# Kernel optimization log

Measured on AMD Instinct MI355X. Metric: run time of the kernel, lower is better.

## Reference

```python
import jax, jax.numpy as jnp
import numpy as np

B, S, T, H, NH, NL = 16, 128, 64, 128, 8, 4
DH = H // NH
FF = 2 * H
SCALE = 1.0 / float(np.sqrt(DH))


def _ln(x, s, b):
    m = x.mean(-1, keepdims=True)
    v = ((x - m) ** 2).mean(-1, keepdims=True)
    return (x - m) * jax.lax.rsqrt(v + 1e-5) * s + b


def _block(x, mask, p):
    Wq, bq, Wk, bk, Wv, bv, Wo, bo, s1, c1, W1, d1, W2, d2, s2, c2 = p
    N, L, _ = x.shape
    q = (x @ Wq + bq).reshape(N, L, NH, DH)
    k = (x @ Wk + bk).reshape(N, L, NH, DH)
    v = (x @ Wv + bv).reshape(N, L, NH, DH)
    scores = jnp.einsum('nqhd,nkhd->nhqk', q, k) * SCALE
    scores = jnp.where(mask[:, None, :, :], scores, -1e9)
    a = jax.nn.softmax(scores, axis=-1)
    o = jnp.einsum('nhqk,nkhd->nqhd', a, v).reshape(N, L, H)
    x = _ln(x + o @ Wo + bo, s1, c1)
    h = jax.nn.relu(x @ W1 + d1)
    return _ln(x + h @ W2 + d2, s2, c2)


def setup_inputs():
    key = jax.random.key(0)
    ks = jax.random.split(key, 16)
    g = lambda k, shape: jax.random.normal(k, shape, jnp.float32) * 0.02
    return {
        'polylines': jax.random.normal(ks[0], (B, S, T, H), jnp.float32),
        'lengths': jax.random.randint(ks[1], (B, S), 0, T + 1),
        'proj_w': g(ks[2], (H, H)), 'proj_b': jnp.zeros((H,), jnp.float32),
        'proj_ln_s': jnp.ones((H,), jnp.float32), 'proj_ln_b': jnp.zeros((H,), jnp.float32),
        'pos_emb': g(ks[3], (1, T, H)),
        'Wq': g(ks[4], (NL, H, H)), 'bq': jnp.zeros((NL, H), jnp.float32),
        'Wk': g(ks[5], (NL, H, H)), 'bk': jnp.zeros((NL, H), jnp.float32),
        'Wv': g(ks[6], (NL, H, H)), 'bv': jnp.zeros((NL, H), jnp.float32),
        'Wo': g(ks[7], (NL, H, H)), 'bo': jnp.zeros((NL, H), jnp.float32),
        'ln1_s': jnp.ones((NL, H), jnp.float32), 'ln1_b': jnp.zeros((NL, H), jnp.float32),
        'W1': g(ks[8], (NL, H, FF)), 'b1': jnp.zeros((NL, FF), jnp.float32),
        'W2': g(ks[9], (NL, FF, H)), 'b2': jnp.zeros((NL, H), jnp.float32),
        'ln2_s': jnp.ones((NL, H), jnp.float32), 'ln2_b': jnp.zeros((NL, H), jnp.float32),
    }


def reference(polylines, lengths, proj_w, proj_b, proj_ln_s, proj_ln_b, pos_emb,
              Wq, bq, Wk, bk, Wv, bv, Wo, bo, ln1_s, ln1_b, W1, b1, W2, b2, ln2_s, ln2_b):
    # valid[b,s,t] = t < lengths[b,s]; lengths==0 -> polyline absent (fully padded)
    valid = jnp.arange(T)[None, None, :] < lengths[:, :, None]  # [B,S,T]
    x = jnp.where(valid[..., None], polylines, -1.0)            # -1 pad as in np.pad(constant_values=-1)
    # mask_temporal[b,s] = outer(valid[b,s], valid[b,s])
    mask_t = (valid[:, :, :, None] & valid[:, :, None, :]).reshape(B * S, T, T)
    # mask_spatial[b,t] = outer(valid[b,:,t], valid[b,:,t])
    vs = jnp.transpose(valid, (0, 2, 1))                        # [B,T,S]
    mask_s = (vs[:, :, :, None] & vs[:, :, None, :]).reshape(B * T, S, S)

    x = x.reshape(B * S, T, H)
    x = jax.nn.relu(_ln(x @ proj_w + proj_b, proj_ln_s, proj_ln_b))  # MLP: Linear->LN->ReLU
    x = x + pos_emb[:, :T, :]

    mask = mask_t
    for i in range(NL):
        if i == NL // 2:
            # switch from temporal to spatial attention: [B*S,T,H] -> [B*T,S,H]
            x = x.reshape(B, S, T, H).transpose(0, 2, 1, 3).reshape(B * T, S, H)
            mask = mask_s
        p = (Wq[i], bq[i], Wk[i], bk[i], Wv[i], bv[i], Wo[i], bo[i],
             ln1_s[i], ln1_b[i], W1[i], b1[i], W2[i], b2[i], ln2_s[i], ln2_b[i])
        x = _block(x, mask, p)
    # faithful to original final reshape (treats [B*T,S,H] buffer as [B,S,T,H])
    return x.reshape(B, S, T, H)[:, 0, :]
```

## Files before the change

### kernel.cpp

```cpp
#include <hip/hip_runtime.h>

typedef short short8 __attribute__((ext_vector_type(8)));
typedef short short4_t __attribute__((ext_vector_type(4)));
typedef float floatx4 __attribute__((ext_vector_type(4)));
typedef unsigned short ushort_t;

#define B_ 16
#define S_ 128
#define T_ 64
#define H_ 128
#define FF_ 256
#define SCALEQK 0.25f

#define OFFP 0
#define OFFQ(l) (16384 + (l) * 65536)
#define OFFK(l) (OFFQ(l) + 16384)
#define OFFV(l) (OFFQ(l) + 32768)
#define OFFO(l) (OFFQ(l) + 49152)
#define OFFW1(l) (278528 + (l) * 65536)
#define OFFW2(l) (OFFW1(l) + 32768)

__device__ __forceinline__ float b2f(ushort_t u) {
    union { unsigned int i; float f; } x; x.i = ((unsigned int)u) << 16; return x.f;
}
__device__ __forceinline__ ushort_t f2b(float f) {
    union { float f; unsigned int i; } x; x.f = f;
    unsigned int r = x.i + 0x7fffu + ((x.i >> 16) & 1u);
    return (ushort_t)(r >> 16);
}
__device__ __forceinline__ int pack2b(float a, float b) {
    return (int)f2b(a) | ((int)f2b(b) << 16);
}

struct WtEnt { const float* src; int N; int K; int nclog2; int dstoff; };
struct WtArgs { WtEnt e[25]; };

__global__ __launch_bounds__(256) void wt_kernel(WtArgs a, ushort_t* __restrict__ dst) {
    WtEnt ent = a.e[blockIdx.x];
    const int tiles_c = ent.N >> 5;
    const int nt = (ent.K >> 5) * tiles_c;
    const int t = blockIdx.y;
    if (t >= nt) return;
    const int tc = t & (tiles_c - 1);
    const int tr = t >> ent.nclog2;
    __shared__ float ld[32 * 33];
    const int tid = threadIdx.x;
#pragma unroll
    for (int i = 0; i < 4; ++i) {
        int e = tid + i * 256;
        int rr = e >> 5, cc = e & 31;
        ld[rr * 33 + cc] = ent.src[(tr * 32 + rr) * ent.N + tc * 32 + cc];
    }
    __syncthreads();
    ushort_t* d = dst + ent.dstoff;
#pragma unroll
    for (int i = 0; i < 4; ++i) {
        int e = tid + i * 256;
        int rr = e >> 5, cc = e & 31;
        d[(tc * 32 + rr) * ent.K + tr * 32 + cc] = f2b(ld[cc * 33 + rr]);
    }
}

template<int RT, int CT, int KK>
__device__ __forceinline__ void mm_g(const ushort_t* aL, int sa,
                                     const ushort_t* __restrict__ wT,
                                     int colbase, int lane, floatx4 (&acc)[RT][CT]) {
    const int l15 = lane & 15, lq8 = (lane >> 4) * 8;
#pragma unroll
    for (int r = 0; r < RT; ++r)
#pragma unroll
        for (int c = 0; c < CT; ++c) acc[r][c] = (floatx4){0.f, 0.f, 0.f, 0.f};
#pragma unroll
    for (int k0 = 0; k0 < KK; k0 += 32) {
        short8 b[CT];
#pragma unroll
        for (int c = 0; c < CT; ++c)
            b[c] = *(const short8*)&wT[(colbase + c * 16 + l15) * KK + k0 + lq8];
#pragma unroll
        for (int r = 0; r < RT; ++r) {
            short8 a = *(const short8*)&aL[(r * 16 + l15) * sa + k0 + lq8];
#pragma unroll
            for (int c = 0; c < CT; ++c)
                acc[r][c] = __builtin_amdgcn_mfma_f32_16x16x32_bf16(a, b[c], acc[r][c], 0, 0, 0);
        }
    }
}

template<int RT, int CT>
__device__ __forceinline__ void add_bias(floatx4 (&acc)[RT][CT], const float* b,
                                         int colbase, int l15) {
#pragma unroll
    for (int c = 0; c < CT; ++c) {
        float bc = b[colbase + c * 16 + l15];
#pragma unroll
        for (int r = 0; r < RT; ++r)
#pragma unroll
            for (int g = 0; g < 4; ++g) acc[r][c][g] += bc;
    }
}

template<int RT, int CT>
__device__ __forceinline__ void add_resid_reg(floatx4 (&acc)[RT][CT],
                                              const float (&res)[RT][CT][4]) {
#pragma unroll
    for (int r = 0; r < RT; ++r)
#pragma unroll
        for (int c = 0; c < CT; ++c)
#pragma unroll
            for (int g = 0; g < 4; ++g) acc[r][c][g] += res[r][c][g];
}
template<int RT, int CT>
__device__ __forceinline__ void save_resid(float (&res)[RT][CT][4],
                                           const floatx4 (&acc)[RT][CT]) {
#pragma unroll
    for (int r = 0; r < RT; ++r)
#pragma unroll
        for (int c = 0; c < CT; ++c)
#pragma unroll
            for (int g = 0; g < 4; ++g) res[r][c][g] = acc[r][c][g];
}

template<int RT, int CT>
__device__ __forceinline__ void st_n(const floatx4 (&acc)[RT][CT], ushort_t* dst, int stride,
                                     int colbase, int l15, int lq) {
#pragma unroll
    for (int r = 0; r < RT; ++r)
#pragma unroll
        for (int g = 0; g < 4; ++g) {
            int row = r * 16 + lq * 4 + g;
#pragma unroll
            for (int c = 0; c < CT; ++c)
                dst[row * stride + colbase + c * 16 + l15] = f2b(acc[r][c][g]);
        }
}

template<int RT, int CT>
__device__ __forceinline__ void st_t(const floatx4 (&acc)[RT][CT], ushort_t* dst, int stride,
                                     int colbase, int l15, int lq) {
#pragma unroll
    for (int r = 0; r < RT; ++r)
#pragma unroll
        for (int c = 0; c < CT; ++c) {
            int d = colbase + c * 16 + l15;
            short4_t p;
#pragma unroll
            for (int g = 0; g < 4; ++g) p[g] = (short)f2b(acc[r][c][g]);
            *(short4_t*)&dst[d * stride + r * 16 + lq * 4] = p;
        }
}

template<int RT, int CT>
__device__ __forceinline__ void ln_norm(floatx4 (&acc)[RT][CT], float* redL,
                                        const float* lns, const float* lnb,
                                        int colbase, int l15, int lq, int wv) {
#pragma unroll
    for (int r = 0; r < RT; ++r)
#pragma unroll
        for (int g = 0; g < 4; ++g) {
            float s = 0.f, q = 0.f;
#pragma unroll
            for (int c = 0; c < CT; ++c) { float v = acc[r][c][g]; s += v; q += v * v; }
            s += __shfl_xor(s, 1); s += __shfl_xor(s, 2); s += __shfl_xor(s, 4); s += __shfl_xor(s, 8);
            q += __shfl_xor(q, 1); q += __shfl_xor(q, 2); q += __shfl_xor(q, 4); q += __shfl_xor(q, 8);
            if (l15 == 0) {
                int row = r * 16 + lq * 4 + g;
                redL[row * 8 + wv] = s;
                redL[row * 8 + 4 + wv] = q;
            }
        }
    __syncthreads();
#pragma unroll
    for (int r = 0; r < RT; ++r)
#pragma unroll
        for (int g = 0; g < 4; ++g) {
            int row = r * 16 + lq * 4 + g;
            float4 S = *(float4*)&redL[row * 8];
            float4 Q = *(float4*)&redL[row * 8 + 4];
            float mean = (S.x + S.y + S.z + S.w) * (1.f / 128.f);
            float var = (Q.x + Q.y + Q.z + Q.w) * (1.f / 128.f) - mean * mean;
            float rstd = rsqrtf(var + 1e-5f);
#pragma unroll
            for (int c = 0; c < CT; ++c) {
                int col = colbase + c * 16 + l15;
                acc[r][c][g] = (acc[r][c][g] - mean) * rstd * lns[col] + lnb[col];
            }
        }
}

template<int JT>
__device__ __forceinline__ void softmax_pack(floatx4 (&st)[JT], bool iv, unsigned jm,
                                             int (&px)[JT][2]) {
    float ev[JT][4];
    float mx = -3.0e38f;
#pragma unroll
    for (int jt = 0; jt < JT; ++jt)
#pragma unroll
        for (int g = 0; g < 4; ++g) {
            bool ok = iv && ((jm >> (jt * 4 + g)) & 1u);
            float s = ok ? st[jt][g] * SCALEQK : -1e9f;
            ev[jt][g] = s; mx = fmaxf(mx, s);
        }
    mx = fmaxf(mx, __shfl_xor(mx, 16)); mx = fmaxf(mx, __shfl_xor(mx, 32));
    float sum = 0.f;
#pragma unroll
    for (int jt = 0; jt < JT; ++jt)
#pragma unroll
        for (int g = 0; g < 4; ++g) { float e = __expf(ev[jt][g] - mx); ev[jt][g] = e; sum += e; }
    sum += __shfl_xor(sum, 16); sum += __shfl_xor(sum, 32);
    float inv = 1.f / sum;
#pragma unroll
    for (int jt = 0; jt < JT; ++jt) {
        px[jt][0] = pack2b(ev[jt][0] * inv, ev[jt][1] * inv);
        px[jt][1] = pack2b(ev[jt][2] * inv, ev[jt][3] * inv);
    }
}

__device__ __forceinline__ short8 pfrag(const int (*px)[2], int jc, int lq, int l15) {
    const int jA = (lq & 1) * 32 + l15;
    int a0 = __shfl(px[jc * 2][0], jA);
    int a1 = __shfl(px[jc * 2][1], jA);
    int a2 = __shfl(px[jc * 2][0], jA + 16);
    int a3 = __shfl(px[jc * 2][1], jA + 16);
    int b0 = __shfl(px[jc * 2 + 1][0], jA);
    int b1 = __shfl(px[jc * 2 + 1][1], jA);
    int b2 = __shfl(px[jc * 2 + 1][0], jA + 16);
    int b3 = __shfl(px[jc * 2 + 1][1], jA + 16);
    const bool t = (lq >> 1) != 0;
    union { int4 i; short8 s; } u;
    u.i = make_int4(t ? b0 : a0, t ? b1 : a1, t ? b2 : a2, t ? b3 : a3);
    return u.s;
}
__device__ __forceinline__ short8 vfrag(const ushort_t* vT, int stride, int row, int off) {
    int2 a = *(const int2*)&vT[row * stride + off];
    int2 b = *(const int2*)&vT[row * stride + off + 4];
    union { int4 i; short8 s; } u;
    u.i = make_int4(a.x, a.y, b.x, b.y);
    return u.s;
}

__global__ __launch_bounds__(256, 2) void k1_mega(
    const float* __restrict__ poly, const int* __restrict__ lens,
    const ushort_t* __restrict__ wt,
    const float* __restrict__ projb, const float* __restrict__ pls,
    const float* __restrict__ plb, const float* __restrict__ pos,
    const float* __restrict__ bq0, const float* __restrict__ bk0,
    const float* __restrict__ bv0, const float* __restrict__ bo0,
    const float* __restrict__ l1s0, const float* __restrict__ l1b0,
    const float* __restrict__ b10, const float* __restrict__ b20,
    const float* __restrict__ l2s0, const float* __restrict__ l2b0,
    const float* __restrict__ bq1, const float* __restrict__ bk1,
    const float* __restrict__ bv1,
    ushort_t* __restrict__ o1, float* __restrict__ xr0f)
{
    __shared__ ushort_t pool[34816];
    __shared__ float redL[512];
    __shared__ float psL[8 * 68];
    __shared__ float q1L[128];
    ushort_t* xL = pool;
    ushort_t* qL = pool + 8704;
    ushort_t* kL = pool + 17408;
    ushort_t* vT = pool + 26112;
    ushort_t* hL = pool + 17408;

    const int tid = threadIdx.x, lane = tid & 63, wv = tid >> 6;
    const int l15 = lane & 15, lq = lane >> 4;
    const int g = blockIdx.x;
    const int len = lens[g];

    {
        const float* pg = poly + (size_t)g * 8192;
#pragma unroll
        for (int it = 0; it < 8; ++it) {
            int e4 = (tid + it * 256) * 4;
            int row = e4 >> 7, col = e4 & 127;
            float4 f = *(const float4*)(pg + e4);
            if (row >= len) { f.x = -1.f; f.y = -1.f; f.z = -1.f; f.w = -1.f; }
            short4_t u;
            u[0] = (short)f2b(f.x); u[1] = (short)f2b(f.y);
            u[2] = (short)f2b(f.z); u[3] = (short)f2b(f.w);
            *(short4_t*)&xL[row * 136 + col] = u;
        }
    }
    __syncthreads();

    floatx4 a2[4][2];
    float xre[4][2][4];

    mm_g<4, 2, 128>(xL, 136, wt + OFFP, wv * 32, lane, a2);
    add_bias<4, 2>(a2, projb, wv * 32, l15);
    ln_norm<4, 2>(a2, redL, pls, plb, wv * 32, l15, lq, wv);
    __syncthreads();
#pragma unroll
    for (int r = 0; r < 4; ++r)
#pragma unroll
        for (int gg = 0; gg < 4; ++gg) {
            int row = r * 16 + lq * 4 + gg;
#pragma unroll
            for (int c = 0; c < 2; ++c) {
                int col = wv * 32 + c * 16 + l15;
                float v = fmaxf(a2[r][c][gg], 0.f) + pos[row * 128 + col];
                xre[r][c][gg] = v;
                xL[row * 136 + col] = f2b(v);
            }
        }
    __syncthreads();

    mm_g<4, 2, 128>(xL, 136, wt + OFFQ(0), wv * 32, lane, a2);
    add_bias<4, 2>(a2, bq0, wv * 32, l15);
    st_n<4, 2>(a2, qL, 136, wv * 32, l15, lq);
    mm_g<4, 2, 128>(xL, 136, wt + OFFK(0), wv * 32, lane, a2);
    add_bias<4, 2>(a2, bk0, wv * 32, l15);
    st_n<4, 2>(a2, kL, 136, wv * 32, l15, lq);
    mm_g<4, 2, 128>(xL, 136, wt + OFFV(0), wv * 32, lane, a2);
    add_bias<4, 2>(a2, bv0, wv * 32, l15);
    st_t<4, 2>(a2, vT, 68, wv * 32, l15, lq);
    __syncthreads();

    {
        const int iRow = wv * 16 + l15;
        const bool iv = iRow < len;
        unsigned jm = 0;
#pragma unroll
        for (int jt = 0; jt < 4; ++jt)
#pragma unroll
            for (int gg = 0; gg < 4; ++gg)
                if (jt * 16 + lq * 4 + gg < len) jm |= (1u << (jt * 4 + gg));
        for (int h = 0; h < 8; ++h) {
            const int hc = h * 16;
            short8 z8 = {0, 0, 0, 0, 0, 0, 0, 0};
            short8 bqf = z8;
            if (lq < 2) bqf = *(const short8*)&qL[iRow * 136 + hc + lq * 8];
            floatx4 st[4];
#pragma unroll
            for (int jt = 0; jt < 4; ++jt) {
                short8 ak = z8;
                if (lq < 2) ak = *(const short8*)&kL[(jt * 16 + l15) * 136 + hc + lq * 8];
                floatx4 zz = {0.f, 0.f, 0.f, 0.f};
                st[jt] = __builtin_amdgcn_mfma_f32_16x16x32_bf16(ak, bqf, zz, 0, 0, 0);
            }
            int px[4][2];
            softmax_pack<4>(st, iv, jm, px);
            floatx4 ao = {0.f, 0.f, 0.f, 0.f};
#pragma unroll
            for (int jc = 0; jc < 2; ++jc) {
                short8 av = vfrag(vT, 68, hc + l15, jc * 32 + lq * 8);
                short8 bp = pfrag(px, jc, lq, l15);
                ao = __builtin_amdgcn_mfma_f32_16x16x32_bf16(av, bp, ao, 0, 0, 0);
            }
            short4_t w;
#pragma unroll
            for (int gg = 0; gg < 4; ++gg) w[gg] = (short)f2b(ao[gg]);
            *(short4_t*)&qL[iRow * 136 + hc + lq * 4] = w;
        }
    }
    __syncthreads();

    mm_g<4, 2, 128>(qL, 136, wt + OFFO(0), wv * 32, lane, a2);
    add_bias<4, 2>(a2, bo0, wv * 32, l15);
    add_resid_reg<4, 2>(a2, xre);
    ln_norm<4, 2>(a2, redL, l1s0, l1b0, wv * 32, l15, lq, wv);
    save_resid<4, 2>(xre, a2);
    st_n<4, 2>(a2, xL, 136, wv * 32, l15, lq);
    __syncthreads();

    {
        floatx4 a4[4][4];
        mm_g<4, 4, 128>(xL, 136, wt + OFFW1(0), wv * 64, lane, a4);
        add_bias<4, 4>(a4, b10, wv * 64, l15);
#pragma unroll
        for (int r = 0; r < 4; ++r)
#pragma unroll
            for (int c = 0; c < 4; ++c)
#pragma unroll
                for (int gg = 0; gg < 4; ++gg) a4[r][c][gg] = fmaxf(a4[r][c][gg], 0.f);
        st_n<4, 4>(a4, hL, 272, wv * 64, l15, lq);
    }
    __syncthreads();

    mm_g<4, 2, 256>(hL, 272, wt + OFFW2(0), wv * 32, lane, a2);
    add_bias<4, 2>(a2, b20, wv * 32, l15);
    add_resid_reg<4, 2>(a2, xre);
    ln_norm<4, 2>(a2, redL, l2s0, l2b0, wv * 32, l15, lq, wv);
    save_resid<4, 2>(xre, a2);
    st_n<4, 2>(a2, xL, 136, wv * 32, l15, lq);
    if (lq == 0) {
#pragma unroll
        for (int c = 0; c < 2; ++c)
            xr0f[(size_t)g * 128 + wv * 32 + c * 16 + l15] = a2[0][c][0];
    }
    __syncthreads();

    mm_g<4, 2, 128>(xL, 136, wt + OFFK(1), wv * 32, lane, a2);
    add_bias<4, 2>(a2, bk1, wv * 32, l15);
    st_n<4, 2>(a2, kL, 136, wv * 32, l15, lq);
    mm_g<4, 2, 128>(xL, 136, wt + OFFV(1), wv * 32, lane, a2);
    add_bias<4, 2>(a2, bv1, wv * 32, l15);
    st_t<4, 2>(a2, vT, 68, wv * 32, l15, lq);
    if (tid < 128) {
        int d = tid;
        float a = bq1[d];
        const ushort_t* wq = wt + OFFQ(1) + d * 128;
#pragma unroll 4
        for (int j0 = 0; j0 < 128; j0 += 8) {
            short8 w8 = *(const short8*)&wq[j0];
            short8 x8 = *(const short8*)&xL[j0];
#pragma unroll
            for (int q = 0; q < 8; ++q)
                a = fmaf(b2f((ushort_t)x8[q]), b2f((ushort_t)w8[q]), a);
        }
        q1L[d] = a;
    }
    __syncthreads();

    {
        int h = tid >> 5, jj = tid & 31;
        int hc = h * 16;
        float s[2];
#pragma unroll
        for (int half = 0; half < 2; ++half) {
            int j = jj + half * 32;
            float a = 0.f;
            short8 k0v = *(const short8*)&kL[j * 136 + hc];
            short8 k1v = *(const short8*)&kL[j * 136 + hc + 8];
#pragma unroll
            for (int q = 0; q < 8; ++q) {
                a = fmaf(q1L[hc + q], b2f((ushort_t)k0v[q]), a);
                a = fmaf(q1L[hc + 8 + q], b2f((ushort_t)k1v[q]), a);
            }
            s[half] = (j < len) ? a * SCALEQK : -1e9f;
        }
        float mx = fmaxf(s[0], s[1]);
#pragma unroll
        for (int d = 1; d < 32; d <<= 1) mx = fmaxf(mx, __shfl_xor(mx, d));
        float e0 = __expf(s[0] - mx), e1 = __expf(s[1] - mx);
        float sum = e0 + e1;
#pragma unroll
        for (int d = 1; d < 32; d <<= 1) sum += __shfl_xor(sum, d);
        float inv = 1.f / sum;
        psL[h * 68 + jj] = e0 * inv;
        psL[h * 68 + jj + 32] = e1 * inv;
    }
    __syncthreads();
    if (tid < 128) {
        int h = tid >> 4, d = tid & 15, hc = h * 16;
        float a = 0.f;
#pragma unroll 4
        for (int j0 = 0; j0 < 64; j0 += 4) {
            float4 p4 = *(const float4*)&psL[h * 68 + j0];
            short4_t v4 = *(const short4_t*)&vT[(hc + d) * 68 + j0];
            a += p4.x * b2f((ushort_t)v4[0]) + p4.y * b2f((ushort_t)v4[1])
               + p4.z * b2f((ushort_t)v4[2]) + p4.w * b2f((ushort_t)v4[3]);
        }
        o1[(size_t)g * 128 + hc + d] = f2b(a);
    }
}

__global__ __launch_bounds__(256, 1) void k2_tail(
    const int* __restrict__ lens, const ushort_t* __restrict__ wt,
    const ushort_t* __restrict__ o1, const float* __restrict__ xr0f,
    const float* __restrict__ bq, const float* __restrict__ bk,
    const float* __restrict__ bv, const float* __restrict__ bo,
    const float* __restrict__ l1s, const float* __restrict__ l1b,
    const float* __restrict__ b1, const float* __restrict__ b2,
    const float* __restrict__ l2s, const float* __restrict__ l2b,
    float* __restrict__ outp)
{
    __shared__ ushort_t pool[69632];
    __shared__ float redL[1024];
    __shared__ int vld[128];
    ushort_t* yL = pool;
    ushort_t* qL = pool + 17408;
    ushort_t* kL = pool + 34816;
    ushort_t* vT = pool + 52224;
    ushort_t* hL = pool + 34816;

    const int tid = threadIdx.x, lane = tid & 63, wv = tid >> 6;
    const int l15 = lane & 15, lq = lane >> 4;
    const int b = blockIdx.x;

    if (tid < 128) vld[tid] = (lens[b * 128 + tid] > 0) ? 1 : 0;
#pragma unroll
    for (int it = 0; it < 8; ++it) {
        int e = tid + it * 256;
        int row = e >> 4, cg = e & 15;
        *(short8*)&kL[row * 136 + cg * 8] =
            *(const short8*)&o1[((size_t)b * 128 + row) * 128 + cg * 8];
    }
    __syncthreads();

    floatx4 a2[8][2];
    float yre[8][2][4];

    mm_g<8, 2, 128>(kL, 136, wt + OFFO(1), wv * 32, lane, a2);
    add_bias<8, 2>(a2, bo + 128, wv * 32, l15);
#pragma unroll
    for (int r = 0; r < 8; ++r)
#pragma unroll
        for (int gg = 0; gg < 4; ++gg) {
            int row = r * 16 + lq * 4 + gg;
#pragma unroll
            for (int c = 0; c < 2; ++c)
                a2[r][c][gg] += xr0f[((size_t)b * 128 + row) * 128 + wv * 32 + c * 16 + l15];
        }
    ln_norm<8, 2>(a2, redL, l1s + 128, l1b + 128, wv * 32, l15, lq, wv);
    save_resid<8, 2>(yre, a2);
    st_n<8, 2>(a2, yL, 136, wv * 32, l15, lq);
    __syncthreads();
    {
        floatx4 a4[8][4];
        mm_g<8, 4, 128>(yL, 136, wt + OFFW1(1), wv * 64, lane, a4);
        add_bias<8, 4>(a4, b1 + FF_, wv * 64, l15);
#pragma unroll
        for (int r = 0; r < 8; ++r)
#pragma unroll
            for (int c = 0; c < 4; ++c)
#pragma unroll
                for (int gg = 0; gg < 4; ++gg) a4[r][c][gg] = fmaxf(a4[r][c][gg], 0.f);
        st_n<8, 4>(a4, hL, 272, wv * 64, l15, lq);
    }
    __syncthreads();
    mm_g<8, 2, 256>(hL, 272, wt + OFFW2(1), wv * 32, lane, a2);
    add_bias<8, 2>(a2, b2 + 128, wv * 32, l15);
    add_resid_reg<8, 2>(a2, yre);
    ln_norm<8, 2>(a2, redL, l2s + 128, l2b + 128, wv * 32, l15, lq, wv);
    save_resid<8, 2>(yre, a2);
    st_n<8, 2>(a2, yL, 136, wv * 32, l15, lq);
    __syncthreads();

    unsigned jm = 0;
#pragma unroll
    for (int jt = 0; jt < 8; ++jt)
#pragma unroll
        for (int gg = 0; gg < 4; ++gg)
            if (vld[jt * 16 + lq * 4 + gg]) jm |= (1u << (jt * 4 + gg));
    const int i0 = wv * 32 + l15, i1 = i0 + 16;
    const bool iv0 = vld[i0] != 0, iv1 = vld[i1] != 0;

    for (int l = 2; l < 4; ++l) {
        mm_g<8, 2, 128>(yL, 136, wt + OFFQ(l), wv * 32, lane, a2);
        add_bias<8, 2>(a2, bq + l * 128, wv * 32, l15);
        st_n<8, 2>(a2, qL, 136, wv * 32, l15, lq);
        mm_g<8, 2, 128>(yL, 136, wt + OFFK(l), wv * 32, lane, a2);
        add_bias<8, 2>(a2, bk + l * 128, wv * 32, l15);
        st_n<8, 2>(a2, kL, 136, wv * 32, l15, lq);
        mm_g<8, 2, 128>(yL, 136, wt + OFFV(l), wv * 32, lane, a2);
        add_bias<8, 2>(a2, bv + l * 128, wv * 32, l15);
        st_t<8, 2>(a2, vT, 136, wv * 32, l15, lq);
        __syncthreads();
        for (int h = 0; h < 8; ++h) {
            const int hc = h * 16;
            short8 z8 = {0, 0, 0, 0, 0, 0, 0, 0};
            short8 bqa = z8, bqb = z8;
            if (lq < 2) {
                bqa = *(const short8*)&qL[i0 * 136 + hc + lq * 8];
                bqb = *(const short8*)&qL[i1 * 136 + hc + lq * 8];
            }
            floatx4 s0[8], s1[8];
#pragma unroll
            for (int jt = 0; jt < 8; ++jt) {
                short8 ak = z8;
                if (lq < 2) ak = *(const short8*)&kL[(jt * 16 + l15) * 136 + hc + lq * 8];
                floatx4 zz = {0.f, 0.f, 0.f, 0.f};
                s0[jt] = __builtin_amdgcn_mfma_f32_16x16x32_bf16(ak, bqa, zz, 0, 0, 0);
                s1[jt] = __builtin_amdgcn_mfma_f32_16x16x32_bf16(ak, bqb, zz, 0, 0, 0);
            }
            int px0[8][2], px1[8][2];
            softmax_pack<8>(s0, iv0, jm, px0);
            softmax_pack<8>(s1, iv1, jm, px1);
            floatx4 o0 = {0.f, 0.f, 0.f, 0.f}, o1a = {0.f, 0.f, 0.f, 0.f};
#pragma unroll
            for (int jc = 0; jc < 4; ++jc) {
                short8 av = vfrag(vT, 136, hc + l15, jc * 32 + lq * 8);
                o0 = __builtin_amdgcn_mfma_f32_16x16x32_bf16(av, pfrag(px0, jc, lq, l15), o0, 0, 0, 0);
                o1a = __builtin_amdgcn_mfma_f32_16x16x32_bf16(av, pfrag(px1, jc, lq, l15), o1a, 0, 0, 0);
            }
            short4_t w0, w1;
#pragma unroll
            for (int gg = 0; gg < 4; ++gg) { w0[gg] = (short)f2b(o0[gg]); w1[gg] = (short)f2b(o1a[gg]); }
            *(short4_t*)&qL[i0 * 136 + hc + lq * 4] = w0;
            *(short4_t*)&qL[i1 * 136 + hc + lq * 4] = w1;
        }
        __syncthreads();
        mm_g<8, 2, 128>(qL, 136, wt + OFFO(l), wv * 32, lane, a2);
        add_bias<8, 2>(a2, bo + l * 128, wv * 32, l15);
        add_resid_reg<8, 2>(a2, yre);
        ln_norm<8, 2>(a2, redL, l1s + l * 128, l1b + l * 128, wv * 32, l15, lq, wv);
        save_resid<8, 2>(yre, a2);
        st_n<8, 2>(a2, yL, 136, wv * 32, l15, lq);
        __syncthreads();
        {
            floatx4 a4[8][4];
            mm_g<8, 4, 128>(yL, 136, wt + OFFW1(l), wv * 64, lane, a4);
            add_bias<8, 4>(a4, b1 + l * FF_, wv * 64, l15);
#pragma unroll
            for (int r = 0; r < 8; ++r)
#pragma unroll
                for (int c = 0; c < 4; ++c)
#pragma unroll
                    for (int gg = 0; gg < 4; ++gg) a4[r][c][gg] = fmaxf(a4[r][c][gg], 0.f);
            st_n<8, 4>(a4, hL, 272, wv * 64, l15, lq);
        }
        __syncthreads();
        mm_g<8, 2, 256>(hL, 272, wt + OFFW2(l), wv * 32, lane, a2);
        add_bias<8, 2>(a2, b2 + l * 128, wv * 32, l15);
        add_resid_reg<8, 2>(a2, yre);
        ln_norm<8, 2>(a2, redL, l2s + l * 128, l2b + l * 128, wv * 32, l15, lq, wv);
        if (l == 3) {
#pragma unroll
            for (int r = 0; r < 4; ++r)
#pragma unroll
                for (int gg = 0; gg < 4; ++gg) {
                    int row = r * 16 + lq * 4 + gg;
#pragma unroll
                    for (int c = 0; c < 2; ++c)
                        outp[(size_t)b * 8192 + row * 128 + wv * 32 + c * 16 + l15] = a2[r][c][gg];
                }
        } else {
            save_resid<8, 2>(yre, a2);
            st_n<8, 2>(a2, yL, 136, wv * 32, l15, lq);
        }
        __syncthreads();
    }
}

extern "C" void kernel_launch(void* const* d_in, const int* in_sizes, int n_in,
                              void* d_out, int out_size, void* d_ws, size_t ws_size,
                              hipStream_t stream)
{
    const float* poly   = (const float*)d_in[0];
    const int*   lens   = (const int*)d_in[1];
    const float* proj_w = (const float*)d_in[2];
    const float* proj_b = (const float*)d_in[3];
    const float* pls    = (const float*)d_in[4];
    const float* plb    = (const float*)d_in[5];
    const float* pos    = (const float*)d_in[6];
    const float* Wq = (const float*)d_in[7];
    const float* bq = (const float*)d_in[8];
    const float* Wk = (const float*)d_in[9];
    const float* bk = (const float*)d_in[10];
    const float* Wv = (const float*)d_in[11];
    const float* bv = (const float*)d_in[12];
    const float* Wo = (const float*)d_in[13];
    const float* bo = (const float*)d_in[14];
    const float* l1s = (const float*)d_in[15];
    const float* l1b = (const float*)d_in[16];
    const float* W1 = (const float*)d_in[17];
    const float* b1 = (const float*)d_in[18];
    const float* W2 = (const float*)d_in[19];
    const float* b2 = (const float*)d_in[20];
    const float* l2s = (const float*)d_in[21];
    const float* l2b = (const float*)d_in[22];
    float* outp = (float*)d_out;

    char* base = (char*)d_ws;
    ushort_t* wt    = (ushort_t*)base;
    ushort_t* o1buf = (ushort_t*)(base + 1081344);
    float* xr0f     = (float*)(base + 1605632);

    const int HH = H_ * H_, HF = H_ * FF_;
    WtArgs wa;
    wa.e[0] = {proj_w, 128, 128, 2, OFFP};
    for (int l = 0; l < 4; ++l) {
        wa.e[1 + l * 4 + 0] = {Wq + l * HH, 128, 128, 2, OFFQ(l)};
        wa.e[1 + l * 4 + 1] = {Wk + l * HH, 128, 128, 2, OFFK(l)};
        wa.e[1 + l * 4 + 2] = {Wv + l * HH, 128, 128, 2, OFFV(l)};
        wa.e[1 + l * 4 + 3] = {Wo + l * HH, 128, 128, 2, OFFO(l)};
    }
    for (int l = 0; l < 4; ++l) {
        wa.e[17 + l * 2 + 0] = {W1 + l * HF, 256, 128, 3, OFFW1(l)};
        wa.e[17 + l * 2 + 1] = {W2 + l * HF, 128, 256, 2, OFFW2(l)};
    }
    wt_kernel<<<dim3(25, 32), 256, 0, stream>>>(wa, wt);

    k1_mega<<<dim3(2048), 256, 0, stream>>>(
        poly, lens, wt,
        proj_b, pls, plb, pos,
        bq, bk, bv, bo, l1s, l1b, b1, b2, l2s, l2b,
        bq + H_, bk + H_, bv + H_,
        o1buf, xr0f);

    k2_tail<<<dim3(16), 256, 0, stream>>>(
        lens, wt, o1buf, xr0f,
        bq, bk, bv, bo, l1s, l1b, b1, b2, l2s, l2b,
        outp);
}
```

Baseline: 471.6 us.

## Prefetch next weight fragments into registers across GEMMs in tail kernel

The 16-block tail kernel now loads each wave's B-operand weight fragments for the next GEMM into registers (double-buffered cur/nxt) while the current GEMM runs on MFMA. The FF GEMMs are split into 128-column and 128-deep chunks so each chunk uses the same fragment shape. This targets global-memory latency on weight loads in a latency-bound kernel with very few blocks. In exchange it needs many more VGPRs (two 8x short8 fragment sets plus accumulators), which could cause spills.

New measurement: 496.3 us. 1.05x slower.

```diff
diff --git a/kernel.cpp b/kernel.cpp
--- a/kernel.cpp
+++ b/kernel.cpp
@@ -236,6 +236,47 @@
     union { int4 i; short8 s; } u;
     u.i = make_int4(a.x, a.y, b.x, b.y);
     return u.s;
+}
+
+struct BFrag { short8 b[8]; };
+__device__ __forceinline__ void ld_bf(BFrag& f, const ushort_t* __restrict__ wT,
+                                      int KK, int colbase, int koff, int lane) {
+    const int l15 = lane & 15, lq8 = (lane >> 4) * 8;
+#pragma unroll
+    for (int c = 0; c < 2; ++c)
+#pragma unroll
+        for (int k = 0; k < 4; ++k)
+            f.b[c * 4 + k] =
+                *(const short8*)&wT[(size_t)(colbase + c * 16 + l15) * KK + koff + k * 32 + lq8];
+}
+template<bool INIT>
+__device__ __forceinline__ void mm_c(const ushort_t* aL, int sa, int aoff,
+                                     const BFrag& f, int lane, floatx4 (&acc)[8][2]) {
+    const int l15 = lane & 15, lq8 = (lane >> 4) * 8;
+    if (INIT) {
+#pragma unroll
+        for (int r = 0; r < 8; ++r)
+#pragma unroll
+            for (int c = 0; c < 2; ++c) acc[r][c] = (floatx4){0.f, 0.f, 0.f, 0.f};
+    }
+#pragma unroll
+    for (int k0 = 0; k0 < 4; ++k0)
+#pragma unroll
+        for (int r = 0; r < 8; ++r) {
+            short8 a = *(const short8*)&aL[(r * 16 + l15) * sa + aoff + k0 * 32 + lq8];
+#pragma unroll
+            for (int c = 0; c < 2; ++c)
+                acc[r][c] = __builtin_amdgcn_mfma_f32_16x16x32_bf16(a, f.b[c * 4 + k0], acc[r][c], 0, 0, 0);
+        }
+}
+template<int RT, int CT>
+__device__ __forceinline__ void relu_a(floatx4 (&acc)[RT][CT]) {
+#pragma unroll
+    for (int r = 0; r < RT; ++r)
+#pragma unroll
+        for (int c = 0; c < CT; ++c)
+#pragma unroll
+            for (int g = 0; g < 4; ++g) acc[r][c][g] = fmaxf(acc[r][c][g], 0.f);
 }
 
 __global__ __launch_bounds__(256, 2) void k1_mega(
@@ -264,11 +305,11 @@
 
     const int tid = threadIdx.x, lane = tid & 63, wv = tid >> 6;
     const int l15 = lane & 15, lq = lane >> 4;
-    const int g = blockIdx.x;
-    const int len = lens[g];
+    const int gid = blockIdx.x;
+    const int len = lens[gid];
 
     {
-        const float* pg = poly + (size_t)g * 8192;
+        const float* pg = poly + (size_t)gid * 8192;
 #pragma unroll
         for (int it = 0; it < 8; ++it) {
             int e4 = (tid + it * 256) * 4;
@@ -367,12 +408,7 @@
         floatx4 a4[4][4];
         mm_g<4, 4, 128>(xL, 136, wt + OFFW1(0), wv * 64, lane, a4);
         add_bias<4, 4>(a4, b10, wv * 64, l15);
-#pragma unroll
-        for (int r = 0; r < 4; ++r)
-#pragma unroll
-            for (int c = 0; c < 4; ++c)
-#pragma unroll
-                for (int gg = 0; gg < 4; ++gg) a4[r][c][gg] = fmaxf(a4[r][c][gg], 0.f);
+        relu_a<4, 4>(a4);
         st_n<4, 4>(a4, hL, 272, wv * 64, l15, lq);
     }
     __syncthreads();
@@ -386,7 +422,7 @@
     if (lq == 0) {
 #pragma unroll
         for (int c = 0; c < 2; ++c)
-            xr0f[(size_t)g * 128 + wv * 32 + c * 16 + l15] = a2[0][c][0];
+            xr0f[(size_t)gid * 128 + wv * 32 + c * 16 + l15] = a2[0][c][0];
     }
     __syncthreads();
 
@@ -451,11 +487,11 @@
             a += p4.x * b2f((ushort_t)v4[0]) + p4.y * b2f((ushort_t)v4[1])
                + p4.z * b2f((ushort_t)v4[2]) + p4.w * b2f((ushort_t)v4[3]);
         }
-        o1[(size_t)g * 128 + hc + d] = f2b(a);
-    }
-}
-
-__global__ __launch_bounds__(256, 1) void k2_tail(
+        o1[(size_t)gid * 128 + hc + d] = f2b(a);
+    }
+}
+
+__global__ __launch_bounds__(256, 1) void k2_pipe(
     const int* __restrict__ lens, const ushort_t* __restrict__ wt,
     const ushort_t* __restrict__ o1, const float* __restrict__ xr0f,
     const float* __restrict__ bq, const float* __restrict__ bk,
@@ -477,6 +513,10 @@
     const int tid = threadIdx.x, lane = tid & 63, wv = tid >> 6;
     const int l15 = lane & 15, lq = lane >> 4;
     const int b = blockIdx.x;
+    const int cb = wv * 32;
+
+    BFrag cur, nxt;
+    ld_bf(cur, wt + OFFO(1), 128, cb, 0, lane);
 
     if (tid < 128) vld[tid] = (lens[b * 128 + tid] > 0) ? 1 : 0;
 #pragma unroll
@@ -491,8 +531,9 @@
     floatx4 a2[8][2];
     float yre[8][2][4];
 
-    mm_g<8, 2, 128>(kL, 136, wt + OFFO(1), wv * 32, lane, a2);
-    add_bias<8, 2>(a2, bo + 128, wv * 32, l15);
+    ld_bf(nxt, wt + OFFW1(1), 128, cb, 0, lane);
+    mm_c<true>(kL, 136, 0, cur, lane, a2);
+    add_bias<8, 2>(a2, bo + H_, cb, l15);
 #pragma unroll
     for (int r = 0; r < 8; ++r)
 #pragma unroll
@@ -500,32 +541,39 @@
             int row = r * 16 + lq * 4 + gg;
 #pragma unroll
             for (int c = 0; c < 2; ++c)
-                a2[r][c][gg] += xr0f[((size_t)b * 128 + row) * 128 + wv * 32 + c * 16 + l15];
-        }
-    ln_norm<8, 2>(a2, redL, l1s + 128, l1b + 128, wv * 32, l15, lq, wv);
+                a2[r][c][gg] += xr0f[((size_t)b * 128 + row) * 128 + cb + c * 16 + l15];
+        }
+    ln_norm<8, 2>(a2, redL, l1s + H_, l1b + H_, cb, l15, lq, wv);
     save_resid<8, 2>(yre, a2);
-    st_n<8, 2>(a2, yL, 136, wv * 32, l15, lq);
-    __syncthreads();
-    {
-        floatx4 a4[8][4];
-        mm_g<8, 4, 128>(yL, 136, wt + OFFW1(1), wv * 64, lane, a4);
-        add_bias<8, 4>(a4, b1 + FF_, wv * 64, l15);
-#pragma unroll
-        for (int r = 0; r < 8; ++r)
-#pragma unroll
-            for (int c = 0; c < 4; ++c)
-#pragma unroll
-                for (int gg = 0; gg < 4; ++gg) a4[r][c][gg] = fmaxf(a4[r][c][gg], 0.f);
-        st_n<8, 4>(a4, hL, 272, wv * 64, l15, lq);
-    }
-    __syncthreads();
-    mm_g<8, 2, 256>(hL, 272, wt + OFFW2(1), wv * 32, lane, a2);
-    add_bias<8, 2>(a2, b2 + 128, wv * 32, l15);
+    st_n<8, 2>(a2, yL, 136, cb, l15, lq);
+    __syncthreads();
+    cur = nxt;
+
+    ld_bf(nxt, wt + OFFW1(1), 128, 128 + cb, 0, lane);
+    mm_c<true>(yL, 136, 0, cur, lane, a2);
+    add_bias<8, 2>(a2, b1 + FF_, cb, l15);
+    relu_a<8, 2>(a2);
+    st_n<8, 2>(a2, hL, 272, cb, l15, lq);
+    cur = nxt;
+    ld_bf(nxt, wt + OFFW2(1), 256, cb, 0, lane);
+    mm_c<true>(yL, 136, 0, cur, lane, a2);
+    add_bias<8, 2>(a2, b1 + FF_, 128 + cb, l15);
+    relu_a<8, 2>(a2);
+    st_n<8, 2>(a2, hL, 272, 128 + cb, l15, lq);
+    __syncthreads();
+    cur = nxt;
+    ld_bf(nxt, wt + OFFW2(1), 256, cb, 128, lane);
+    mm_c<true>(hL, 272, 0, cur, lane, a2);
+    cur = nxt;
+    ld_bf(nxt, wt + OFFQ(2), 128, cb, 0, lane);
+    mm_c<false>(hL, 272, 128, cur, lane, a2);
+    add_bias<8, 2>(a2, b2 + H_, cb, l15);
     add_resid_reg<8, 2>(a2, yre);
-    ln_norm<8, 2>(a2, redL, l2s + 128, l2b + 128, wv * 32, l15, lq, wv);
+    ln_norm<8, 2>(a2, redL, l2s + H_, l2b + H_, cb, l15, lq, wv);
     save_resid<8, 2>(yre, a2);
-    st_n<8, 2>(a2, yL, 136, wv * 32, l15, lq);
-    __syncthreads();
+    st_n<8, 2>(a2, yL, 136, cb, l15, lq);
+    __syncthreads();
+    cur = nxt;
 
     unsigned jm = 0;
 #pragma unroll
@@ -533,20 +581,26 @@
 #pragma unroll
         for (int gg = 0; gg < 4; ++gg)
             if (vld[jt * 16 + lq * 4 + gg]) jm |= (1u << (jt * 4 + gg));
-    const int i0 = wv * 32 + l15, i1 = i0 + 16;
+    const int i0 = cb + l15, i1 = i0 + 16;
     const bool iv0 = vld[i0] != 0, iv1 = vld[i1] != 0;
 
     for (int l = 2; l < 4; ++l) {
-        mm_g<8, 2, 128>(yL, 136, wt + OFFQ(l), wv * 32, lane, a2);
-        add_bias<8, 2>(a2, bq + l * 128, wv * 32, l15);
-        st_n<8, 2>(a2, qL, 136, wv * 32, l15, lq);
-        mm_g<8, 2, 128>(yL, 136, wt + OFFK(l), wv * 32, lane, a2);
-        add_bias<8, 2>(a2, bk + l * 128, wv * 32, l15);
-        st_n<8, 2>(a2, kL, 136, wv * 32, l15, lq);
-        mm_g<8, 2, 128>(yL, 136, wt + OFFV(l), wv * 32, lane, a2);
-        add_bias<8, 2>(a2, bv + l * 128, wv * 32, l15);
-        st_t<8, 2>(a2, vT, 136, wv * 32, l15, lq);
+        ld_bf(nxt, wt + OFFK(l), 128, cb, 0, lane);
+        mm_c<true>(yL, 136, 0, cur, lane, a2);
+        add_bias<8, 2>(a2, bq + l * H_, cb, l15);
+        st_n<8, 2>(a2, qL, 136, cb, l15, lq);
+        cur = nxt;
+        ld_bf(nxt, wt + OFFV(l), 128, cb, 0, lane);
+        mm_c<true>(yL, 136, 0, cur, lane, a2);
+        add_bias<8, 2>(a2, bk + l * H_, cb, l15);
+        st_n<8, 2>(a2, kL, 136, cb, l15, lq);
+        cur = nxt;
+        ld_bf(nxt, wt + OFFO(l), 128, cb, 0, lane);
+        mm_c<true>(yL, 136, 0, cur, lane, a2);
+        add_bias<8, 2>(a2, bv + l * H_, cb, l15);
+        st_t<8, 2>(a2, vT, 136, cb, l15, lq);
         __syncthreads();
+        cur = nxt;
         for (int h = 0; h < 8; ++h) {
             const int hc = h * 16;
             short8 z8 = {0, 0, 0, 0, 0, 0, 0, 0};
@@ -581,31 +635,42 @@
             *(short4_t*)&qL[i1 * 136 + hc + lq * 4] = w1;
         }
         __syncthreads();
-        mm_g<8, 2, 128>(qL, 136, wt + OFFO(l), wv * 32, lane, a2);
-        add_bias<8, 2>(a2, bo + l * 128, wv * 32, l15);
+        ld_bf(nxt, wt + OFFW1(l), 128, cb, 0, lane);
+        mm_c<true>(qL, 136, 0, cur, lane, a2);
+        add_bias<8, 2>(a2, bo + l * H_, cb, l15);
         add_resid_reg<8, 2>(a2, yre);
-        ln_norm<8, 2>(a2, redL, l1s + l * 128, l1b + l * 128, wv * 32, l15, lq, wv);
+        ln_norm<8, 2>(a2, redL, l1s + l * H_, l1b + l * H_, cb, l15, lq, wv);
         save_resid<8, 2>(yre, a2);
-        st_n<8, 2>(a2, yL, 136, wv * 32, l15, lq);
+        st_n<8, 2>(a2, yL, 136, cb, l15, lq);
         __syncthreads();
-        {
-            floatx4 a4[8][4];
-            mm_g<8, 4, 128>(yL, 136, wt + OFFW1(l), wv * 64, lane, a4);
-            add_bias<8, 4>(a4, b1 + l * FF_, wv * 64, l15);
-#pragma unroll
-            for (int r = 0; r < 8; ++r)
-#pragma unroll
-                for (int c = 0; c < 4; ++c)
-#pragma unroll
-                    for (int gg = 0; gg < 4; ++gg) a4[r][c][gg] = fmaxf(a4[r][c][gg], 0.f);
-            st_n<8, 4>(a4, hL, 272, wv * 64, l15, lq);
-        }
+        cur = nxt;
+        ld_bf(nxt, wt + OFFW1(l), 128, 128 + cb, 0, lane);
+        mm_c<true>(yL, 136, 0, cur, lane, a2);
+        add_bias<8, 2>(a2, b1 + l * FF_, cb, l15);
+        relu_a<8, 2>(a2);
+        st_n<8, 2>(a2, hL, 272, cb, l15, lq);
+        cur = nxt;
+        ld_bf(nxt, wt + OFFW2(l), 256, cb, 0, lane);
+        mm_c<true>(yL, 136, 0, cur, lane, a2);
+        add_bias<8, 2>(a2, b1 + l * FF_, 128 + cb, l15);
+        relu_a<8, 2>(a2);
+        st_n<8, 2>(a2, hL, 272, 128 + cb, l15, lq);
         __syncthreads();
-        mm_g<8, 2, 256>(hL, 272, wt + OFFW2(l), wv * 32, lane, a2);
-        add_bias<8, 2>(a2, b2 + l * 128, wv * 32, l15);
+        cur = nxt;
+        ld_bf(nxt, wt + OFFW2(l), 256, cb, 128, lane);
+        mm_c<true>(hL, 272, 0, cur, lane, a2);
+        cur = nxt;
+        if (l == 2) ld_bf(nxt, wt + OFFQ(3), 128, cb, 0, lane);
+        mm_c<false>(hL, 272, 128, cur, lane, a2);
+        add_bias<8, 2>(a2, b2 + l * H_, cb, l15);
         add_resid_reg<8, 2>(a2, yre);
-        ln_norm<8, 2>(a2, redL, l2s + l * 128, l2b + l * 128, wv * 32, l15, lq, wv);
-        if (l == 3) {
+        ln_norm<8, 2>(a2, redL, l2s + l * H_, l2b + l * H_, cb, l15, lq, wv);
+        if (l == 2) {
+            save_resid<8, 2>(yre, a2);
+            st_n<8, 2>(a2, yL, 136, cb, l15, lq);
+            __syncthreads();
+            cur = nxt;
+        } else {
 #pragma unroll
             for (int r = 0; r < 4; ++r)
 #pragma unroll
@@ -613,13 +678,9 @@
                     int row = r * 16 + lq * 4 + gg;
 #pragma unroll
                     for (int c = 0; c < 2; ++c)
-                        outp[(size_t)b * 8192 + row * 128 + wv * 32 + c * 16 + l15] = a2[r][c][gg];
+                        outp[(size_t)b * 8192 + row * 128 + cb + c * 16 + l15] = a2[r][c][gg];
                 }
-        } else {
-            save_resid<8, 2>(yre, a2);
-            st_n<8, 2>(a2, yL, 136, wv * 32, l15, lq);
-        }
-        __syncthreads();
+        }
     }
 }
 
@@ -679,7 +740,7 @@
         bq + H_, bk + H_, bv + H_,
         o1buf, xr0f);
 
-    k2_tail<<<dim3(16), 256, 0, stream>>>(
+    k2_pipe<<<dim3(16), 256, 0, stream>>>(
         lens, wt, o1buf, xr0f,
         bq, bk, bv, bo, l1s, l1b, b1, b2, l2s, l2b,
         outp);
```
